# Performance work log

Measured on AMD Instinct MI355X. Metric: run time of the kernel, lower is better.

Reference implementation:

```python
import jax, jax.numpy as jnp
import numpy as np

D_MODEL = 1024
D_INTERNAL = 64
SEQ = 2048
BATCH = 4


def setup_inputs() -> dict:
    key = jax.random.key(0)
    ks = jax.random.split(key, 9)
    s = 1.0 / np.sqrt(D_MODEL)
    return {
        "query": jax.random.normal(ks[0], (SEQ, BATCH, D_MODEL), jnp.float32),
        "key": jax.random.normal(ks[1], (SEQ, BATCH, D_MODEL), jnp.float32),
        "value": jax.random.normal(ks[2], (SEQ, BATCH, D_MODEL), jnp.float32),
        "Wq": jax.random.normal(ks[3], (D_MODEL, D_INTERNAL), jnp.float32) * s,
        "bq": jnp.zeros((D_INTERNAL,), jnp.float32),
        "Wk": jax.random.normal(ks[4], (D_MODEL, D_INTERNAL), jnp.float32) * s,
        "bk": jnp.zeros((D_INTERNAL,), jnp.float32),
        "Wv": jax.random.normal(ks[5], (D_MODEL, D_MODEL), jnp.float32) * s,
        "bv": jnp.zeros((D_MODEL,), jnp.float32),
    }


def reference(query, key, value, Wq, bq, Wk, bk, Wv, bv):
    # inputs: (S, B, D); project then move batch first -> (B, S, *)
    q = (query @ Wq + bq).transpose(1, 0, 2)          # (B, S, d_int)
    k = (key @ Wk + bk).transpose(1, 0, 2)            # (B, S, d_int)
    v = (value @ Wv + bv).transpose(1, 0, 2)          # (B, S, D)
    scores = jnp.einsum("bqd,bkd->bqk", q, k) / jnp.sqrt(jnp.float32(D_INTERNAL))
    probs = jax.nn.softmax(scores, axis=-1)           # row softmax over keys
    # extra renormalization over the QUERY axis (dim=1), as in the source
    probs = probs / (1e-9 + probs.sum(axis=1, keepdims=True))
    aten = jnp.einsum("bqk,bkd->bqd", probs, v).transpose(1, 0, 2)  # (S, B, D)
    return aten, probs
```

## Files before the change

kernel.cpp:

```cpp
#include <hip/hip_runtime.h>
#include <math.h>

#define SEQ 2048
#define BATCH 4
#define DM 1024
#define DI 64

typedef __attribute__((ext_vector_type(8))) short bf16x8;
typedef __attribute__((ext_vector_type(4))) float f32x4;

__device__ __forceinline__ unsigned short f2bf(float f) {
  unsigned u = __float_as_uint(f);
  unsigned r = (u + 0x7fff + ((u >> 16) & 1)) >> 16;
  return (unsigned short)r;
}

__device__ __forceinline__ void gload_lds16(const void* g, void* l) {
  __builtin_amdgcn_global_load_lds(
      (const __attribute__((address_space(1))) unsigned int*)g,
      (__attribute__((address_space(3))) unsigned int*)l, 16, 0, 0);
}


__global__ __launch_bounds__(256) void wqkt_kernel(
    const float* __restrict__ Wq, const float* __restrict__ Wk,
    unsigned short* __restrict__ WqkT) {
  __shared__ unsigned short t[64][65];
  const float* W = blockIdx.y ? Wk : Wq;
  unsigned short* WT = WqkT + (size_t)blockIdx.y * DI * DM;
  int bx = blockIdx.x * 64;
  int lx = threadIdx.x & 63, ly = threadIdx.x >> 6;
#pragma unroll
  for (int i = 0; i < 64; i += 4)
    t[ly + i][lx] = f2bf(W[(size_t)(bx + ly + i) * DI + lx]);
  __syncthreads();
#pragma unroll
  for (int i = 0; i < 64; i += 4)
    WT[(size_t)(ly + i) * DM + bx + lx] = t[lx][ly + i];
}

__global__ __launch_bounds__(256) void wvt_kernel(
    const float* __restrict__ W, unsigned short* __restrict__ WT) {
  __shared__ unsigned short t[64][65];
  int bx = blockIdx.x * 64, by = blockIdx.y * 64;
  int lx = threadIdx.x & 63, ly = threadIdx.x >> 6;
#pragma unroll
  for (int i = 0; i < 64; i += 4)
    t[ly + i][lx] = f2bf(W[(size_t)(bx + ly + i) * DM + by + lx]);
  __syncthreads();
#pragma unroll
  for (int i = 0; i < 64; i += 4)
    WT[(size_t)(by + ly + i) * DM + bx + lx] = t[lx][ly + i];
}

__global__ __launch_bounds__(256) void qkproj_mfma(
    const float* __restrict__ query, const float* __restrict__ key,
    const unsigned short* __restrict__ WqkT,
    const float* __restrict__ bq, const float* __restrict__ bk,
    unsigned short* __restrict__ qbf, unsigned short* __restrict__ kbf) {
  __shared__ __align__(16) unsigned short As[32 * 32];
  __shared__ __align__(16) unsigned short Bs[64 * 32];
  int which = blockIdx.y;
  const float* A = (which ? key : query) + (size_t)blockIdx.x * 32 * DM;
  const unsigned short* Bt = WqkT + (size_t)which * DI * DM;
  const float* bias = which ? bk : bq;
  unsigned short* outp = which ? kbf : qbf;

  const int tid = threadIdx.x;
  const int lane = tid & 63, wave = tid >> 6;
  const int lrow = lane & 15, quad = lane >> 4;
  const int wr = (wave >> 1) * 16;
  const int wc = (wave & 1) * 32;
  const int sw = (quad ^ ((lrow >> 1) & 3)) * 8;
  f32x4 acc[2] = {};

  const int am = tid >> 3, asub = tid & 7;
  const int akc = asub * 4;
  const int asl = am * 32 + (((asub >> 1) ^ ((am >> 1) & 3)) * 8) + (asub & 1) * 4;
  const int bn = tid >> 2;
  const int bkc = (((tid & 3) ^ ((bn >> 1) & 3)) * 8);

  for (int k0 = 0; k0 < DM; k0 += 32) {
    __syncthreads();
    gload_lds16(Bt + (size_t)bn * DM + k0 + bkc, Bs + wave * 512);
    float4 a = *(const float4*)(A + (size_t)am * DM + k0 + akc);
    ushort4 h;
    h.x = f2bf(a.x); h.y = f2bf(a.y); h.z = f2bf(a.z); h.w = f2bf(a.w);
    *(ushort4*)&As[asl] = h;
    __syncthreads();
    bf16x8 af = *(const bf16x8*)&As[(wr + lrow) * 32 + sw];
    bf16x8 b0 = *(const bf16x8*)&Bs[(wc + lrow) * 32 + sw];
    bf16x8 b1 = *(const bf16x8*)&Bs[(wc + 16 + lrow) * 32 + sw];
    acc[0] = __builtin_amdgcn_mfma_f32_16x16x32_bf16(af, b0, acc[0], 0, 0, 0);
    acc[1] = __builtin_amdgcn_mfma_f32_16x16x32_bf16(af, b1, acc[1], 0, 0, 0);
  }
  int sbase = blockIdx.x * 8 + (wr >> 2) + quad;
#pragma unroll
  for (int ni = 0; ni < 2; ++ni) {
    int n = wc + ni * 16 + lrow;
    float bb = bias[n];
#pragma unroll
    for (int reg = 0; reg < 4; ++reg)
      outp[((size_t)reg * SEQ + sbase) * DI + n] = f2bf(acc[ni][reg] + bb);
  }
}

__global__ __launch_bounds__(256) void vcast_kernel(
    const float* __restrict__ value, unsigned short* __restrict__ vbf) {
  size_t i = ((size_t)blockIdx.x * 256 + threadIdx.x) * 8;
  float4 a = *(const float4*)(value + i);
  float4 b = *(const float4*)(value + i + 4);
  bf16x8 h;
  h[0] = (short)f2bf(a.x); h[1] = (short)f2bf(a.y);
  h[2] = (short)f2bf(a.z); h[3] = (short)f2bf(a.w);
  h[4] = (short)f2bf(b.x); h[5] = (short)f2bf(b.y);
  h[6] = (short)f2bf(b.z); h[7] = (short)f2bf(b.w);
  *(bf16x8*)(vbf + i) = h;
}

__device__ __forceinline__ void mfma_core_bb(
    const unsigned short* __restrict__ At, int lda,
    const unsigned short* __restrict__ Bt, int ldb,
    int K, f32x4 (&acc)[4][4],
    unsigned short* As, unsigned short* Bs) {
  const int tid  = threadIdx.x;
  const int lane = tid & 63;
  const int wave = tid >> 6;
  const int wr   = (wave >> 1) * 64;
  const int wc   = (wave & 1) * 64;
  const int lrow = lane & 15;
  const int quad = lane >> 4;
  const int sw   = (quad ^ ((lrow >> 1) & 3)) * 8;

  for (int k0 = 0; k0 < K; k0 += 32) {
    __syncthreads();
#pragma unroll
    for (int it = 0; it < 2; ++it) {
      int c = it * 256 + wave * 64 + lane;
      int m = c >> 2, kc = ((c & 3) ^ ((c >> 3) & 3)) * 8;
      gload_lds16(At + (size_t)m * lda + k0 + kc,
                  As + (size_t)(it * 256 + wave * 64) * 8);
    }
#pragma unroll
    for (int it = 0; it < 2; ++it) {
      int c = it * 256 + wave * 64 + lane;
      int n = c >> 2, kc = ((c & 3) ^ ((c >> 3) & 3)) * 8;
      gload_lds16(Bt + (size_t)n * ldb + k0 + kc,
                  Bs + (size_t)(it * 256 + wave * 64) * 8);
    }
    __syncthreads();
    bf16x8 af[4], bfr[4];
#pragma unroll
    for (int mi = 0; mi < 4; ++mi)
      af[mi] = *(const bf16x8*)&As[(wr + mi * 16 + lrow) * 32 + sw];
#pragma unroll
    for (int ni = 0; ni < 4; ++ni)
      bfr[ni] = *(const bf16x8*)&Bs[(wc + ni * 16 + lrow) * 32 + sw];
#pragma unroll
    for (int mi = 0; mi < 4; ++mi)
#pragma unroll
      for (int ni = 0; ni < 4; ++ni)
        acc[mi][ni] = __builtin_amdgcn_mfma_f32_16x16x32_bf16(
            af[mi], bfr[ni], acc[mi][ni], 0, 0, 0);
  }
}

__device__ __forceinline__ void mfma_core_bb_12864(
    const unsigned short* __restrict__ At, int lda,
    const unsigned short* __restrict__ Bt, int ldb,
    int K, f32x4 (&acc)[4][2],
    unsigned short* As, unsigned short* Bs) {
  const int tid  = threadIdx.x;
  const int lane = tid & 63;
  const int wave = tid >> 6;
  const int wr   = (wave >> 1) * 64;
  const int wc   = (wave & 1) * 32;
  const int lrow = lane & 15;
  const int quad = lane >> 4;
  const int sw   = (quad ^ ((lrow >> 1) & 3)) * 8;
  const int bn   = tid >> 2;
  const int bkc  = ((tid & 3) ^ ((bn >> 1) & 3)) * 8;

  for (int k0 = 0; k0 < K; k0 += 32) {
    __syncthreads();
#pragma unroll
    for (int it = 0; it < 2; ++it) {
      int c = it * 256 + tid;
      int m = c >> 2, kc = ((c & 3) ^ ((m >> 1) & 3)) * 8;
      gload_lds16(At + (size_t)m * lda + k0 + kc,
                  As + (size_t)(it * 256 + wave * 64) * 8);
    }
    gload_lds16(Bt + (size_t)bn * ldb + k0 + bkc, Bs + wave * 512);
    __syncthreads();
    bf16x8 af[4], bfr[2];
#pragma unroll
    for (int mi = 0; mi < 4; ++mi)
      af[mi] = *(const bf16x8*)&As[(wr + mi * 16 + lrow) * 32 + sw];
#pragma unroll
    for (int ni = 0; ni < 2; ++ni)
      bfr[ni] = *(const bf16x8*)&Bs[(wc + ni * 16 + lrow) * 32 + sw];
#pragma unroll
    for (int mi = 0; mi < 4; ++mi)
#pragma unroll
      for (int ni = 0; ni < 2; ++ni)
        acc[mi][ni] = __builtin_amdgcn_mfma_f32_16x16x32_bf16(
            af[mi], bfr[ni], acc[mi][ni], 0, 0, 0);
  }
}

__global__ __launch_bounds__(256) void vproj_mfma(
    const unsigned short* __restrict__ vbf, const unsigned short* __restrict__ WvT,
    const float* __restrict__ bv, unsigned short* __restrict__ vT) {
  __shared__ __align__(16) unsigned short As[128 * 32];
  __shared__ __align__(16) unsigned short Bs[64 * 32];
  __shared__ __align__(16) unsigned short ep[64 * 4 * 32];
  f32x4 acc[4][2] = {};
  int m0 = blockIdx.x * 128, n0 = blockIdx.y * 64;
  mfma_core_bb_12864(vbf + (size_t)m0 * DM, DM, WvT + (size_t)n0 * DM, DM, DM,
                     acc, As, Bs);
  const int tid = threadIdx.x;
  const int lane = tid & 63, wave = tid >> 6;
  const int wr = (wave >> 1) * 64, wc = (wave & 1) * 32;
  const int lrow = lane & 15, quad = lane >> 4;
#pragma unroll
  for (int mi = 0; mi < 4; ++mi) {
    int ss = (wr >> 2) + mi * 4 + quad;
#pragma unroll
    for (int ni = 0; ni < 2; ++ni) {
      int nn = wc + ni * 16 + lrow;
      float bias = bv[n0 + nn];
      int swz = (nn & 3) << 3;
#pragma unroll
      for (int reg = 0; reg < 4; ++reg)
        ep[nn * 128 + reg * 32 + (ss ^ swz)] = f2bf(acc[mi][ni][reg] + bias);
    }
  }
  __syncthreads();
  int s0 = m0 >> 2;
#pragma unroll
  for (int t8 = 0; t8 < 4; ++t8) {
    int c = t8 * 256 + tid;
    int ss8 = (c & 3) * 8, b = (c >> 2) & 3, nn = c >> 4;
    uint4 vv = *(const uint4*)&ep[nn * 128 + b * 32 + (ss8 ^ ((nn & 3) << 3))];
    *(uint4*)&vT[((size_t)(b * DM + n0 + nn)) * SEQ + s0 + ss8] = vv;
  }
}

__global__ __launch_bounds__(256) void scores_mfma(
    const unsigned short* __restrict__ qbf, const unsigned short* __restrict__ kbf,
    float* __restrict__ probs, float* __restrict__ rowsum) {
  __shared__ __align__(16) unsigned short As[128 * 32];
  __shared__ __align__(16) unsigned short Bs[128 * 32];
  int b = blockIdx.z;
  f32x4 acc[4][4] = {};
  mfma_core_bb(qbf + ((size_t)b * SEQ + blockIdx.x * 128) * DI, DI,
               kbf + ((size_t)b * SEQ + blockIdx.y * 128) * DI, DI, DI,
               acc, As, Bs);
  float* C = probs + (size_t)b * SEQ * SEQ;
  float* rs = rowsum + (size_t)b * SEQ;
  const int lane = threadIdx.x & 63, wave = threadIdx.x >> 6;
  const int wr = (wave >> 1) * 64, wc = (wave & 1) * 64;
  const int lrow = lane & 15, quad = lane >> 4;
#pragma unroll
  for (int mi = 0; mi < 4; ++mi) {
    int qr = blockIdx.x * 128 + wr + mi * 16 + quad * 4;
    float r0 = 0.f, r1 = 0.f, r2 = 0.f, r3 = 0.f;
#pragma unroll
    for (int ni = 0; ni < 4; ++ni) {
      int n = blockIdx.y * 128 + wc + ni * 16 + lrow;
      float e0 = __expf(acc[mi][ni][0] * 0.125f);
      float e1 = __expf(acc[mi][ni][1] * 0.125f);
      float e2 = __expf(acc[mi][ni][2] * 0.125f);
      float e3 = __expf(acc[mi][ni][3] * 0.125f);
      C[(size_t)(qr + 0) * SEQ + n] = e0;
      C[(size_t)(qr + 1) * SEQ + n] = e1;
      C[(size_t)(qr + 2) * SEQ + n] = e2;
      C[(size_t)(qr + 3) * SEQ + n] = e3;
      r0 += e0; r1 += e1; r2 += e2; r3 += e3;
    }
    r0 += __shfl_xor(r0, 1); r0 += __shfl_xor(r0, 2);
    r0 += __shfl_xor(r0, 4); r0 += __shfl_xor(r0, 8);
    r1 += __shfl_xor(r1, 1); r1 += __shfl_xor(r1, 2);
    r1 += __shfl_xor(r1, 4); r1 += __shfl_xor(r1, 8);
    r2 += __shfl_xor(r2, 1); r2 += __shfl_xor(r2, 2);
    r2 += __shfl_xor(r2, 4); r2 += __shfl_xor(r2, 8);
    r3 += __shfl_xor(r3, 1); r3 += __shfl_xor(r3, 2);
    r3 += __shfl_xor(r3, 4); r3 += __shfl_xor(r3, 8);
    if (lrow == 0) {
      atomicAdd(&rs[qr + 0], r0);
      atomicAdd(&rs[qr + 1], r1);
      atomicAdd(&rs[qr + 2], r2);
      atomicAdd(&rs[qr + 3], r3);
    }
  }
}

__global__ void zero_kernel(float* __restrict__ p, int n) {
  int i = blockIdx.x * blockDim.x + threadIdx.x;
  if (i < n) p[i] = 0.f;
}

__global__ void recip_kernel(const float* __restrict__ in,
                             float* __restrict__ outp, float eps, int n) {
  int i = blockIdx.x * blockDim.x + threadIdx.x;
  if (i < n) outp[i] = 1.0f / (eps + in[i]);
}

__global__ __launch_bounds__(256) void colsum_kernel(
    const float* __restrict__ probs, const float* __restrict__ invrs,
    float* __restrict__ colsum) {
  int b = blockIdx.z;
  int k = blockIdx.x * 256 + threadIdx.x;
  int q0 = blockIdx.y * 128;
  const float* p = probs + (size_t)b * SEQ * SEQ + (size_t)q0 * SEQ + k;
  const float* ir = invrs + (size_t)b * SEQ + q0;
  float sum = 0.f;
#pragma unroll 4
  for (int i = 0; i < 128; ++i) sum += p[(size_t)i * SEQ] * ir[i];
  atomicAdd(&colsum[b * SEQ + k], sum);
}

__global__ __launch_bounds__(256) void renorm_kernel(
    float* __restrict__ probs, const float* __restrict__ invrs,
    const float* __restrict__ invcol, unsigned short* __restrict__ smb) {
  size_t i4 = (size_t)blockIdx.x * blockDim.x + threadIdx.x;
  size_t f = i4 * 4;
  int b = (int)(f >> 22);
  int q = (int)((f >> 11) & 2047);
  int k = (int)(f & 2047);
  float ir = invrs[b * SEQ + q];
  float4 p = *(float4*)(probs + f);
  float4 c = *(const float4*)(invcol + b * SEQ + k);
  p.x *= ir * c.x; p.y *= ir * c.y; p.z *= ir * c.z; p.w *= ir * c.w;
  *(float4*)(probs + f) = p;
  ushort4 h;
  h.x = f2bf(p.x); h.y = f2bf(p.y); h.z = f2bf(p.z); h.w = f2bf(p.w);
  *(ushort4*)(smb + f) = h;
}

__global__ __launch_bounds__(256) void aten_mfma(
    const unsigned short* __restrict__ smb, const unsigned short* __restrict__ vT,
    float* __restrict__ out) {
  __shared__ __align__(16) unsigned short As[128 * 32];
  __shared__ __align__(16) unsigned short Bs[128 * 32];
  int bid = blockIdx.x;
  int wg = (bid & 7) * 64 + (bid >> 3);
  int mb = wg & 15, nb = (wg >> 4) & 7, b = wg >> 7;
  f32x4 acc[4][4] = {};
  int m0 = mb * 128, n0 = nb * 128;
  mfma_core_bb(smb + ((size_t)b * SEQ + m0) * SEQ, SEQ,
               vT + ((size_t)b * DM + n0) * SEQ, SEQ, SEQ, acc, As, Bs);
  const int lane = threadIdx.x & 63, wave = threadIdx.x >> 6;
  const int wr = (wave >> 1) * 64, wc = (wave & 1) * 64;
  const int lrow = lane & 15, quad = lane >> 4;
#pragma unroll
  for (int mi = 0; mi < 4; ++mi) {
    int qr = m0 + wr + mi * 16 + quad * 4;
#pragma unroll
    for (int ni = 0; ni < 4; ++ni) {
      int n = n0 + wc + ni * 16 + lrow;
#pragma unroll
      for (int reg = 0; reg < 4; ++reg)
        out[(size_t)(qr + reg) * (BATCH * DM) + b * DM + n] = acc[mi][ni][reg];
    }
  }
}

extern "C" void kernel_launch(void* const* d_in, const int* in_sizes, int n_in,
                              void* d_out, int out_size, void* d_ws, size_t ws_size,
                              hipStream_t stream) {
  const float* query = (const float*)d_in[0];
  const float* key   = (const float*)d_in[1];
  const float* value = (const float*)d_in[2];
  const float* Wq    = (const float*)d_in[3];
  const float* bq    = (const float*)d_in[4];
  const float* Wk    = (const float*)d_in[5];
  const float* bk    = (const float*)d_in[6];
  const float* Wv    = (const float*)d_in[7];
  const float* bv    = (const float*)d_in[8];

  float* out   = (float*)d_out;
  float* probs = out + (size_t)SEQ * BATCH * DM;

  unsigned short* WvT  = (unsigned short*)d_ws;
  unsigned short* WqkT = WvT  + (size_t)DM * DM;
  unsigned short* qbf  = WqkT + (size_t)2 * DI * DM;
  unsigned short* kbf  = qbf  + (size_t)BATCH * SEQ * DI;
  unsigned short* vT   = kbf  + (size_t)BATCH * SEQ * DI;
  unsigned short* smb  = vT   + (size_t)BATCH * DM * SEQ;
  unsigned short* vbf  = smb;
  float* rowsum = (float*)(smb + (size_t)BATCH * SEQ * SEQ);
  float* colsum = rowsum + (size_t)BATCH * SEQ;
  float* invrs  = colsum + (size_t)BATCH * SEQ;
  float* invcol = invrs  + (size_t)BATCH * SEQ;

  wqkt_kernel<<<dim3(16, 2), 256, 0, stream>>>(Wq, Wk, WqkT);
  qkproj_mfma<<<dim3(SEQ * BATCH / 32, 2), 256, 0, stream>>>(
      query, key, WqkT, bq, bk, qbf, kbf);
  wvt_kernel<<<dim3(16, 16), 256, 0, stream>>>(Wv, WvT);
  vcast_kernel<<<(SEQ * BATCH * DM / 8) / 256, 256, 0, stream>>>(value, vbf);
  vproj_mfma<<<dim3(SEQ * BATCH / 128, DM / 64), 256, 0, stream>>>(vbf, WvT, bv, vT);
  zero_kernel<<<(2 * BATCH * SEQ + 255) / 256, 256, 0, stream>>>(rowsum, 2 * BATCH * SEQ);
  scores_mfma<<<dim3(SEQ / 128, SEQ / 128, BATCH), 256, 0, stream>>>(
      qbf, kbf, probs, rowsum);
  recip_kernel<<<(BATCH * SEQ + 255) / 256, 256, 0, stream>>>(
      rowsum, invrs, 0.0f, BATCH * SEQ);
  colsum_kernel<<<dim3(SEQ / 256, SEQ / 128, BATCH), 256, 0, stream>>>(
      probs, invrs, colsum);
  recip_kernel<<<(BATCH * SEQ + 255) / 256, 256, 0, stream>>>(
      colsum, invcol, 1e-9f, BATCH * SEQ);
  renorm_kernel<<<(BATCH * SEQ * SEQ / 4) / 256, 256, 0, stream>>>(
      probs, invrs, invcol, smb);
  aten_mfma<<<dim3(512), 256, 0, stream>>>(smb, vT, out);
}
```

Before: 335.1 us.

## Fuse probability renormalization into the attention-output GEMM A-tile load

The separate renorm pass, which read probs, wrote the fp32 probs and a bf16 copy, is removed. The final GEMM now loads the fp32 exp scores straight from a scratch buffer, applies the row and column inverse scales in registers, converts to bf16 into LDS, and writes one k-slice of the final probs per N-block. This drops a full read-modify-write of the 64 MB probs tensor and the bf16 intermediate. In exchange, each of the eight N-blocks rereads the fp32 A tile, doubling A traffic compared with bf16. The A load is also no longer async and no longer pipelined.

```diff
diff --git a/kernel.cpp b/kernel.cpp
--- a/kernel.cpp
+++ b/kernel.cpp
@@ -248,7 +248,7 @@
 
 __global__ __launch_bounds__(256) void scores_mfma(
     const unsigned short* __restrict__ qbf, const unsigned short* __restrict__ kbf,
-    float* __restrict__ probs, float* __restrict__ rowsum) {
+    float* __restrict__ escr, float* __restrict__ rowsum) {
   __shared__ __align__(16) unsigned short As[128 * 32];
   __shared__ __align__(16) unsigned short Bs[128 * 32];
   int b = blockIdx.z;
@@ -256,7 +256,7 @@
   mfma_core_bb(qbf + ((size_t)b * SEQ + blockIdx.x * 128) * DI, DI,
                kbf + ((size_t)b * SEQ + blockIdx.y * 128) * DI, DI, DI,
                acc, As, Bs);
-  float* C = probs + (size_t)b * SEQ * SEQ;
+  float* C = escr + (size_t)b * SEQ * SEQ;
   float* rs = rowsum + (size_t)b * SEQ;
   const int lane = threadIdx.x & 63, wave = threadIdx.x >> 6;
   const int wr = (wave >> 1) * 64, wc = (wave & 1) * 64;
@@ -307,12 +307,12 @@
 }
 
 __global__ __launch_bounds__(256) void colsum_kernel(
-    const float* __restrict__ probs, const float* __restrict__ invrs,
+    const float* __restrict__ escr, const float* __restrict__ invrs,
     float* __restrict__ colsum) {
   int b = blockIdx.z;
   int k = blockIdx.x * 256 + threadIdx.x;
   int q0 = blockIdx.y * 128;
-  const float* p = probs + (size_t)b * SEQ * SEQ + (size_t)q0 * SEQ + k;
+  const float* p = escr + (size_t)b * SEQ * SEQ + (size_t)q0 * SEQ + k;
   const float* ir = invrs + (size_t)b * SEQ + q0;
   float sum = 0.f;
 #pragma unroll 4
@@ -320,39 +320,70 @@
   atomicAdd(&colsum[b * SEQ + k], sum);
 }
 
-__global__ __launch_bounds__(256) void renorm_kernel(
-    float* __restrict__ probs, const float* __restrict__ invrs,
-    const float* __restrict__ invcol, unsigned short* __restrict__ smb) {
-  size_t i4 = (size_t)blockIdx.x * blockDim.x + threadIdx.x;
-  size_t f = i4 * 4;
-  int b = (int)(f >> 22);
-  int q = (int)((f >> 11) & 2047);
-  int k = (int)(f & 2047);
-  float ir = invrs[b * SEQ + q];
-  float4 p = *(float4*)(probs + f);
-  float4 c = *(const float4*)(invcol + b * SEQ + k);
-  p.x *= ir * c.x; p.y *= ir * c.y; p.z *= ir * c.z; p.w *= ir * c.w;
-  *(float4*)(probs + f) = p;
-  ushort4 h;
-  h.x = f2bf(p.x); h.y = f2bf(p.y); h.z = f2bf(p.z); h.w = f2bf(p.w);
-  *(ushort4*)(smb + f) = h;
-}
-
-__global__ __launch_bounds__(256) void aten_mfma(
-    const unsigned short* __restrict__ smb, const unsigned short* __restrict__ vT,
-    float* __restrict__ out) {
+__global__ __launch_bounds__(256) void aten_fused(
+    const float* __restrict__ escr, const unsigned short* __restrict__ vT,
+    const float* __restrict__ invrs, const float* __restrict__ invcol,
+    float* __restrict__ probs, float* __restrict__ out) {
   __shared__ __align__(16) unsigned short As[128 * 32];
   __shared__ __align__(16) unsigned short Bs[128 * 32];
+  __shared__ float irs[128];
   int bid = blockIdx.x;
   int wg = (bid & 7) * 64 + (bid >> 3);
-  int mb = wg & 15, nb = (wg >> 4) & 7, b = wg >> 7;
-  f32x4 acc[4][4] = {};
+  int nb = wg & 7, mb = (wg >> 3) & 15, b = wg >> 7;
   int m0 = mb * 128, n0 = nb * 128;
-  mfma_core_bb(smb + ((size_t)b * SEQ + m0) * SEQ, SEQ,
-               vT + ((size_t)b * DM + n0) * SEQ, SEQ, SEQ, acc, As, Bs);
-  const int lane = threadIdx.x & 63, wave = threadIdx.x >> 6;
+  const float* A = escr + ((size_t)b * SEQ + m0) * SEQ;
+  const unsigned short* Bt = vT + ((size_t)b * DM + n0) * SEQ;
+  const float* ic = invcol + (size_t)b * SEQ;
+  float* P = probs + ((size_t)b * SEQ + m0) * SEQ;
+
+  const int tid = threadIdx.x;
+  const int lane = tid & 63, wave = tid >> 6;
   const int wr = (wave >> 1) * 64, wc = (wave & 1) * 64;
   const int lrow = lane & 15, quad = lane >> 4;
+  const int sw = (quad ^ ((lrow >> 1) & 3)) * 8;
+  const int klo = nb * 256;
+
+  if (tid < 128) irs[tid] = invrs[(size_t)b * SEQ + m0 + tid];
+
+  f32x4 acc[4][4] = {};
+  for (int k0 = 0; k0 < SEQ; k0 += 32) {
+    __syncthreads();
+#pragma unroll
+    for (int it = 0; it < 2; ++it) {
+      int c = it * 256 + wave * 64 + lane;
+      int n = c >> 2, kc = ((c & 3) ^ ((c >> 3) & 3)) * 8;
+      gload_lds16(Bt + (size_t)n * SEQ + k0 + kc,
+                  Bs + (size_t)(it * 256 + wave * 64) * 8);
+    }
+    bool wp = (unsigned)(k0 - klo) < 256u;
+#pragma unroll
+    for (int it = 0; it < 4; ++it) {
+      int c = it * 256 + tid;
+      int m = c >> 3, asub = c & 7, kc = asub * 4;
+      float4 a = *(const float4*)(A + (size_t)m * SEQ + k0 + kc);
+      float s = irs[m];
+      float4 c4 = *(const float4*)(ic + k0 + kc);
+      a.x *= s * c4.x; a.y *= s * c4.y; a.z *= s * c4.z; a.w *= s * c4.w;
+      if (wp) *(float4*)(P + (size_t)m * SEQ + k0 + kc) = a;
+      ushort4 h;
+      h.x = f2bf(a.x); h.y = f2bf(a.y); h.z = f2bf(a.z); h.w = f2bf(a.w);
+      *(ushort4*)&As[m * 32 + (((asub >> 1) ^ ((m >> 1) & 3)) * 8) + (asub & 1) * 4] = h;
+    }
+    __syncthreads();
+    bf16x8 af[4], bfr[4];
+#pragma unroll
+    for (int mi = 0; mi < 4; ++mi)
+      af[mi] = *(const bf16x8*)&As[(wr + mi * 16 + lrow) * 32 + sw];
+#pragma unroll
+    for (int ni = 0; ni < 4; ++ni)
+      bfr[ni] = *(const bf16x8*)&Bs[(wc + ni * 16 + lrow) * 32 + sw];
+#pragma unroll
+    for (int mi = 0; mi < 4; ++mi)
+#pragma unroll
+      for (int ni = 0; ni < 4; ++ni)
+        acc[mi][ni] = __builtin_amdgcn_mfma_f32_16x16x32_bf16(
+            af[mi], bfr[ni], acc[mi][ni], 0, 0, 0);
+  }
 #pragma unroll
   for (int mi = 0; mi < 4; ++mi) {
     int qr = m0 + wr + mi * 16 + quad * 4;
@@ -387,9 +418,9 @@
   unsigned short* qbf  = WqkT + (size_t)2 * DI * DM;
   unsigned short* kbf  = qbf  + (size_t)BATCH * SEQ * DI;
   unsigned short* vT   = kbf  + (size_t)BATCH * SEQ * DI;
-  unsigned short* smb  = vT   + (size_t)BATCH * DM * SEQ;
-  unsigned short* vbf  = smb;
-  float* rowsum = (float*)(smb + (size_t)BATCH * SEQ * SEQ);
+  float* escr = (float*)(vT + (size_t)BATCH * DM * SEQ);
+  unsigned short* vbf  = (unsigned short*)escr;
+  float* rowsum = escr + (size_t)BATCH * SEQ * SEQ;
   float* colsum = rowsum + (size_t)BATCH * SEQ;
   float* invrs  = colsum + (size_t)BATCH * SEQ;
   float* invcol = invrs  + (size_t)BATCH * SEQ;
@@ -402,14 +433,12 @@
   vproj_mfma<<<dim3(SEQ * BATCH / 128, DM / 64), 256, 0, stream>>>(vbf, WvT, bv, vT);
   zero_kernel<<<(2 * BATCH * SEQ + 255) / 256, 256, 0, stream>>>(rowsum, 2 * BATCH * SEQ);
   scores_mfma<<<dim3(SEQ / 128, SEQ / 128, BATCH), 256, 0, stream>>>(
-      qbf, kbf, probs, rowsum);
+      qbf, kbf, escr, rowsum);
   recip_kernel<<<(BATCH * SEQ + 255) / 256, 256, 0, stream>>>(
       rowsum, invrs, 0.0f, BATCH * SEQ);
   colsum_kernel<<<dim3(SEQ / 256, SEQ / 128, BATCH), 256, 0, stream>>>(
-      probs, invrs, colsum);
+      escr, invrs, colsum);
   recip_kernel<<<(BATCH * SEQ + 255) / 256, 256, 0, stream>>>(
       colsum, invcol, 1e-9f, BATCH * SEQ);
-  renorm_kernel<<<(BATCH * SEQ * SEQ / 4) / 256, 256, 0, stream>>>(
-      probs, invrs, invcol, smb);
-  aten_mfma<<<dim3(512), 256, 0, stream>>>(smb, vT, out);
-}
+  aten_fused<<<dim3(512), 256, 0, stream>>>(escr, vT, invrs, invcol, probs, out);
+}
```

Result: slower. 377.6 us (+12.7%).

## Store unnormalized exp scores as bf16 and fold normalizations into V and epilogue

Applied to the files above, without the earlier changes.

The scores kernel now writes exp(scores) as bf16 instead of fp32. The column normalization is folded into V by scaling vT per key, and the row normalization is applied in the aten epilogue. The fp32 probs output is written once by a separate kernel that reads the bf16 buffer. This drops the fp32 read-modify-write renorm pass and halves score traffic, but probs now carry bf16 rounding of the exponentials, which may lower output accuracy.

```diff
diff --git a/kernel.cpp b/kernel.cpp
--- a/kernel.cpp
+++ b/kernel.cpp
@@ -13,6 +13,10 @@
   unsigned u = __float_as_uint(f);
   unsigned r = (u + 0x7fff + ((u >> 16) & 1)) >> 16;
   return (unsigned short)r;
+}
+
+__device__ __forceinline__ float bf2f(unsigned short u) {
+  return __uint_as_float((unsigned)u << 16);
 }
 
 __device__ __forceinline__ void gload_lds16(const void* g, void* l) {
@@ -248,7 +252,7 @@
 
 __global__ __launch_bounds__(256) void scores_mfma(
     const unsigned short* __restrict__ qbf, const unsigned short* __restrict__ kbf,
-    float* __restrict__ probs, float* __restrict__ rowsum) {
+    unsigned short* __restrict__ ebf, float* __restrict__ rowsum) {
   __shared__ __align__(16) unsigned short As[128 * 32];
   __shared__ __align__(16) unsigned short Bs[128 * 32];
   int b = blockIdx.z;
@@ -256,7 +260,7 @@
   mfma_core_bb(qbf + ((size_t)b * SEQ + blockIdx.x * 128) * DI, DI,
                kbf + ((size_t)b * SEQ + blockIdx.y * 128) * DI, DI, DI,
                acc, As, Bs);
-  float* C = probs + (size_t)b * SEQ * SEQ;
+  unsigned short* C = ebf + (size_t)b * SEQ * SEQ;
   float* rs = rowsum + (size_t)b * SEQ;
   const int lane = threadIdx.x & 63, wave = threadIdx.x >> 6;
   const int wr = (wave >> 1) * 64, wc = (wave & 1) * 64;
@@ -272,10 +276,10 @@
       float e1 = __expf(acc[mi][ni][1] * 0.125f);
       float e2 = __expf(acc[mi][ni][2] * 0.125f);
       float e3 = __expf(acc[mi][ni][3] * 0.125f);
-      C[(size_t)(qr + 0) * SEQ + n] = e0;
-      C[(size_t)(qr + 1) * SEQ + n] = e1;
-      C[(size_t)(qr + 2) * SEQ + n] = e2;
-      C[(size_t)(qr + 3) * SEQ + n] = e3;
+      C[(size_t)(qr + 0) * SEQ + n] = f2bf(e0);
+      C[(size_t)(qr + 1) * SEQ + n] = f2bf(e1);
+      C[(size_t)(qr + 2) * SEQ + n] = f2bf(e2);
+      C[(size_t)(qr + 3) * SEQ + n] = f2bf(e3);
       r0 += e0; r1 += e1; r2 += e2; r3 += e3;
     }
     r0 += __shfl_xor(r0, 1); r0 += __shfl_xor(r0, 2);
@@ -307,61 +311,87 @@
 }
 
 __global__ __launch_bounds__(256) void colsum_kernel(
-    const float* __restrict__ probs, const float* __restrict__ invrs,
+    const unsigned short* __restrict__ ebf, const float* __restrict__ invrs,
     float* __restrict__ colsum) {
   int b = blockIdx.z;
   int k = blockIdx.x * 256 + threadIdx.x;
   int q0 = blockIdx.y * 128;
-  const float* p = probs + (size_t)b * SEQ * SEQ + (size_t)q0 * SEQ + k;
+  const unsigned short* p = ebf + (size_t)b * SEQ * SEQ + (size_t)q0 * SEQ + k;
   const float* ir = invrs + (size_t)b * SEQ + q0;
   float sum = 0.f;
 #pragma unroll 4
-  for (int i = 0; i < 128; ++i) sum += p[(size_t)i * SEQ] * ir[i];
+  for (int i = 0; i < 128; ++i) sum += bf2f(p[(size_t)i * SEQ]) * ir[i];
   atomicAdd(&colsum[b * SEQ + k], sum);
 }
 
-__global__ __launch_bounds__(256) void renorm_kernel(
-    float* __restrict__ probs, const float* __restrict__ invrs,
-    const float* __restrict__ invcol, unsigned short* __restrict__ smb) {
-  size_t i4 = (size_t)blockIdx.x * blockDim.x + threadIdx.x;
-  size_t f = i4 * 4;
+__global__ __launch_bounds__(256) void vscale_kernel(
+    unsigned short* __restrict__ vT, const float* __restrict__ invcol) {
+  size_t i = ((size_t)blockIdx.x * 256 + threadIdx.x) * 8;
+  int s = (int)(i & (SEQ - 1));
+  int b = (int)(i >> 21);
+  bf16x8 v = *(const bf16x8*)(vT + i);
+  const float* ic = invcol + (size_t)b * SEQ + s;
+  float4 c0 = *(const float4*)(ic);
+  float4 c1 = *(const float4*)(ic + 4);
+  bf16x8 r;
+  r[0] = (short)f2bf(bf2f((unsigned short)v[0]) * c0.x);
+  r[1] = (short)f2bf(bf2f((unsigned short)v[1]) * c0.y);
+  r[2] = (short)f2bf(bf2f((unsigned short)v[2]) * c0.z);
+  r[3] = (short)f2bf(bf2f((unsigned short)v[3]) * c0.w);
+  r[4] = (short)f2bf(bf2f((unsigned short)v[4]) * c1.x);
+  r[5] = (short)f2bf(bf2f((unsigned short)v[5]) * c1.y);
+  r[6] = (short)f2bf(bf2f((unsigned short)v[6]) * c1.z);
+  r[7] = (short)f2bf(bf2f((unsigned short)v[7]) * c1.w);
+  *(bf16x8*)(vT + i) = r;
+}
+
+__global__ __launch_bounds__(256) void probsout_kernel(
+    const unsigned short* __restrict__ ebf, const float* __restrict__ invrs,
+    const float* __restrict__ invcol, float* __restrict__ probs) {
+  size_t f = ((size_t)blockIdx.x * 256 + threadIdx.x) * 4;
   int b = (int)(f >> 22);
   int q = (int)((f >> 11) & 2047);
   int k = (int)(f & 2047);
+  ushort4 h = *(const ushort4*)(ebf + f);
   float ir = invrs[b * SEQ + q];
-  float4 p = *(float4*)(probs + f);
   float4 c = *(const float4*)(invcol + b * SEQ + k);
-  p.x *= ir * c.x; p.y *= ir * c.y; p.z *= ir * c.z; p.w *= ir * c.w;
+  float4 p;
+  p.x = bf2f(h.x) * ir * c.x;
+  p.y = bf2f(h.y) * ir * c.y;
+  p.z = bf2f(h.z) * ir * c.z;
+  p.w = bf2f(h.w) * ir * c.w;
   *(float4*)(probs + f) = p;
-  ushort4 h;
-  h.x = f2bf(p.x); h.y = f2bf(p.y); h.z = f2bf(p.z); h.w = f2bf(p.w);
-  *(ushort4*)(smb + f) = h;
 }
 
 __global__ __launch_bounds__(256) void aten_mfma(
-    const unsigned short* __restrict__ smb, const unsigned short* __restrict__ vT,
-    float* __restrict__ out) {
+    const unsigned short* __restrict__ ebf, const unsigned short* __restrict__ vT,
+    const float* __restrict__ invrs, float* __restrict__ out) {
   __shared__ __align__(16) unsigned short As[128 * 32];
   __shared__ __align__(16) unsigned short Bs[128 * 32];
+  __shared__ float irs[128];
   int bid = blockIdx.x;
   int wg = (bid & 7) * 64 + (bid >> 3);
   int mb = wg & 15, nb = (wg >> 4) & 7, b = wg >> 7;
+  int m0 = mb * 128, n0 = nb * 128;
+  if (threadIdx.x < 128)
+    irs[threadIdx.x] = invrs[(size_t)b * SEQ + m0 + threadIdx.x];
   f32x4 acc[4][4] = {};
-  int m0 = mb * 128, n0 = nb * 128;
-  mfma_core_bb(smb + ((size_t)b * SEQ + m0) * SEQ, SEQ,
+  mfma_core_bb(ebf + ((size_t)b * SEQ + m0) * SEQ, SEQ,
                vT + ((size_t)b * DM + n0) * SEQ, SEQ, SEQ, acc, As, Bs);
   const int lane = threadIdx.x & 63, wave = threadIdx.x >> 6;
   const int wr = (wave >> 1) * 64, wc = (wave & 1) * 64;
   const int lrow = lane & 15, quad = lane >> 4;
 #pragma unroll
   for (int mi = 0; mi < 4; ++mi) {
-    int qr = m0 + wr + mi * 16 + quad * 4;
+    int rb = wr + mi * 16 + quad * 4;
+    int qr = m0 + rb;
 #pragma unroll
     for (int ni = 0; ni < 4; ++ni) {
       int n = n0 + wc + ni * 16 + lrow;
 #pragma unroll
       for (int reg = 0; reg < 4; ++reg)
-        out[(size_t)(qr + reg) * (BATCH * DM) + b * DM + n] = acc[mi][ni][reg];
+        out[(size_t)(qr + reg) * (BATCH * DM) + b * DM + n] =
+            acc[mi][ni][reg] * irs[rb + reg];
     }
   }
 }
@@ -387,9 +417,9 @@
   unsigned short* qbf  = WqkT + (size_t)2 * DI * DM;
   unsigned short* kbf  = qbf  + (size_t)BATCH * SEQ * DI;
   unsigned short* vT   = kbf  + (size_t)BATCH * SEQ * DI;
-  unsigned short* smb  = vT   + (size_t)BATCH * DM * SEQ;
-  unsigned short* vbf  = smb;
-  float* rowsum = (float*)(smb + (size_t)BATCH * SEQ * SEQ);
+  unsigned short* ebf  = vT   + (size_t)BATCH * DM * SEQ;
+  unsigned short* vbf  = ebf;
+  float* rowsum = (float*)(ebf + (size_t)BATCH * SEQ * SEQ);
   float* colsum = rowsum + (size_t)BATCH * SEQ;
   float* invrs  = colsum + (size_t)BATCH * SEQ;
   float* invcol = invrs  + (size_t)BATCH * SEQ;
@@ -402,14 +432,15 @@
   vproj_mfma<<<dim3(SEQ * BATCH / 128, DM / 64), 256, 0, stream>>>(vbf, WvT, bv, vT);
   zero_kernel<<<(2 * BATCH * SEQ + 255) / 256, 256, 0, stream>>>(rowsum, 2 * BATCH * SEQ);
   scores_mfma<<<dim3(SEQ / 128, SEQ / 128, BATCH), 256, 0, stream>>>(
-      qbf, kbf, probs, rowsum);
+      qbf, kbf, ebf, rowsum);
   recip_kernel<<<(BATCH * SEQ + 255) / 256, 256, 0, stream>>>(
       rowsum, invrs, 0.0f, BATCH * SEQ);
   colsum_kernel<<<dim3(SEQ / 256, SEQ / 128, BATCH), 256, 0, stream>>>(
-      probs, invrs, colsum);
+      ebf, invrs, colsum);
   recip_kernel<<<(BATCH * SEQ + 255) / 256, 256, 0, stream>>>(
       colsum, invcol, 1e-9f, BATCH * SEQ);
-  renorm_kernel<<<(BATCH * SEQ * SEQ / 4) / 256, 256, 0, stream>>>(
-      probs, invrs, invcol, smb);
-  aten_mfma<<<dim3(512), 256, 0, stream>>>(smb, vT, out);
-}
+  vscale_kernel<<<(BATCH * DM * SEQ / 8) / 256, 256, 0, stream>>>(vT, invcol);
+  aten_mfma<<<dim3(512), 256, 0, stream>>>(ebf, vT, invrs, out);
+  probsout_kernel<<<(BATCH * SEQ * SEQ / 4) / 256, 256, 0, stream>>>(
+      ebf, invrs, invcol, probs);
+}
```

Result: no change. 330.2 us (-1.5%).
